# Kernel tuning notes

Measured on AMD Instinct MI355X. Metric: run time of the kernel, lower is better.

The kernel has to match this reference:

```python
import jax, jax.numpy as jnp
import jax.scipy.linalg as jsl
import numpy as np

EPS = 1e-7            # torchvision iou-loss eps
GIOU_THRESHOLD = 0.2
MIN_VARIANCE = 1e-6


def cxcywh_to_xyxy(b):
    cx, cy, w, h = b[..., 0], b[..., 1], b[..., 2], b[..., 3]
    return jnp.stack([cx - 0.5 * w, cy - 0.5 * h, cx + 0.5 * w, cy + 0.5 * h], axis=-1)


def kalman_filtered_boxes(prev_boxes, prev_logits, image_sizes, swp, sws, log_q_diag):
    # scale: [B,1,4] = [w,h,w,h] for denormalization
    scale = jnp.stack([image_sizes[:, 1], image_sizes[:, 0], image_sizes[:, 1], image_sizes[:, 0]], axis=-1)[:, None, :]
    box_abs = prev_boxes * scale                               # [B,Q,4] absolute cxcywh
    conf = jax.nn.softmax(prev_logits, axis=-1).max(axis=-1)   # [B,Q]
    # predict step: P_pred = F P0 F^T + Q  (track-independent 8x8)
    idx = jnp.arange(4)
    F = jnp.eye(8, dtype=box_abs.dtype).at[idx, idx + 4].set(1.0)
    P0 = jnp.diag(jnp.array([100.0] * 4 + [1000.0] * 4, dtype=box_abs.dtype))
    Qm = jnp.diag(jnp.exp(log_q_diag))
    P_pred = F @ P0 @ F.T + Qm                                 # [8,8]
    # detection covariance R per track (DetectionCovarianceGate)
    hc = jnp.maximum(box_abs[..., 3], 1.0)
    std = jnp.stack([swp * hc, swp * hc, sws * hc, sws * hc], axis=-1)
    std = std / jnp.maximum(conf, 1e-6)[..., None]
    std = jnp.maximum(std, 0.1)
    eye4 = jnp.eye(4, dtype=box_abs.dtype)
    R = eye4 * (std ** 2)[..., None, :] + MIN_VARIANCE * eye4  # [B,Q,4,4]
    # innovation covariance, gain via batched Cholesky + triangular solves
    S = P_pred[:4, :4] + R + MIN_VARIANCE * eye4               # [B,Q,4,4]
    L = jnp.linalg.cholesky(S)
    covHT_T = jnp.broadcast_to(P_pred[:, :4].T, S.shape[:-2] + (4, 8))
    y = jsl.solve_triangular(L, covHT_T, lower=True)
    Kt = jsl.solve_triangular(jnp.swapaxes(L, -1, -2), y, lower=False)
    K = jnp.swapaxes(Kt, -1, -2)                               # [B,Q,8,4]
    # state init from the same box + zero velocity -> F @ mean0 = [box; 0]
    mean_pred = jnp.concatenate([box_abs, jnp.zeros_like(box_abs)], axis=-1)  # [B,Q,8]
    innovation = box_abs - mean_pred[..., :4]  # identically zero; kept faithful to original
    mean_new = mean_pred + jnp.einsum('bqij,bqj->bqi', K, innovation)
    return mean_new[..., :4] / scale


def pairwise_giou_loss(p, t):
    # p: [B,Q,4], t: [B,T,4] in xyxy -> [B,Q,T] GIoU loss
    a = p[:, :, None, :]
    b = t[:, None, :, :]
    area_a = (a[..., 2] - a[..., 0]) * (a[..., 3] - a[..., 1])
    area_b = (b[..., 2] - b[..., 0]) * (b[..., 3] - b[..., 1])
    lt = jnp.maximum(a[..., :2], b[..., :2])
    rb = jnp.minimum(a[..., 2:], b[..., 2:])
    wh = jnp.maximum(rb - lt, 0.0)
    inter = wh[..., 0] * wh[..., 1]
    union = area_a + area_b - inter
    iou = inter / (union + EPS)
    ltc = jnp.minimum(a[..., :2], b[..., :2])
    rbc = jnp.maximum(a[..., 2:], b[..., 2:])
    whc = jnp.maximum(rbc - ltc, 0.0)
    area_c = whc[..., 0] * whc[..., 1]
    giou = iou - (area_c - union) / (area_c + EPS)
    return 1.0 - giou


def ciou_loss_mean(p, t):
    # elementwise complete-IoU loss (torchvision semantics), mean-reduced
    x1, y1, x2, y2 = p[..., 0], p[..., 1], p[..., 2], p[..., 3]
    xg1, yg1, xg2, yg2 = t[..., 0], t[..., 1], t[..., 2], t[..., 3]
    iw = jnp.maximum(jnp.minimum(x2, xg2) - jnp.maximum(x1, xg1), 0.0)
    ih = jnp.maximum(jnp.minimum(y2, yg2) - jnp.maximum(y1, yg1), 0.0)
    inter = iw * ih
    union = (x2 - x1) * (y2 - y1) + (xg2 - xg1) * (yg2 - yg1) - inter
    iou = inter / (union + EPS)
    cw = jnp.maximum(x2, xg2) - jnp.minimum(x1, xg1)
    ch = jnp.maximum(y2, yg2) - jnp.minimum(y1, yg1)
    c2 = cw ** 2 + ch ** 2 + EPS
    d2 = ((x1 + x2 - xg1 - xg2) ** 2 + (y1 + y2 - yg1 - yg2) ** 2) / 4.0
    v = (4.0 / (jnp.pi ** 2)) * (jnp.arctan((xg2 - xg1) / (yg2 - yg1)) - jnp.arctan((x2 - x1) / (y2 - y1))) ** 2
    alpha = jax.lax.stop_gradient(v / (1.0 - iou + v + EPS))
    return jnp.mean(1.0 - iou + d2 / c2 + alpha * v)


def _hungarian(cost):
    # O(n^3) shortest-augmenting-path Hungarian (min-cost square assignment).
    # Returns col assignment for rows 0..n-1 (rows are implicitly arange(n)).
    n = cost.shape[0]
    u = np.zeros(n + 1)
    v = np.zeros(n + 1)
    p = np.zeros(n + 1, dtype=np.int64)
    way = np.zeros(n + 1, dtype=np.int64)
    for i in range(1, n + 1):
        p[0] = i
        j0 = 0
        minv = np.full(n + 1, np.inf)
        used = np.zeros(n + 1, dtype=bool)
        while True:
            used[j0] = True
            i0 = p[j0]
            js = np.nonzero(~used)[0]
            js = js[js > 0]
            cur = cost[i0 - 1, js - 1] - u[i0] - v[js]
            upd = cur < minv[js]
            minv[js] = np.minimum(minv[js], cur)
            way[js[upd]] = j0
            j1 = js[int(np.argmin(minv[js]))]
            delta = minv[j1]
            uj = np.nonzero(used)[0]
            u[p[uj]] += delta
            v[uj] -= delta
            minv[js] -= delta
            j0 = j1
            if p[j0] == 0:
                break
        while j0 != 0:
            j1 = way[j0]
            p[j0] = p[j1]
            j0 = j1
    col_of_row = np.empty(n, dtype=np.int64)
    for j in range(1, n + 1):
        col_of_row[p[j] - 1] = j - 1
    return col_of_row


def setup_inputs() -> dict:
    key = jax.random.key(0)
    k = jax.random.split(key, 4)
    B, Q, C = 8, 512, 92
    prev_boxes = jax.random.uniform(k[0], (B, Q, 4), jnp.float32)
    prev_logits = jax.random.normal(k[1], (B, Q, C), jnp.float32)
    curr_boxes = jax.random.uniform(k[2], (B, Q, 4), jnp.float32)
    image_sizes = jax.random.uniform(k[3], (B, 2), jnp.float32) * 800.0 + 480.0
    return {
        'prev_boxes': prev_boxes,
        'prev_logits': prev_logits,
        'curr_boxes': curr_boxes,
        'image_sizes': image_sizes,
        'std_weight_position': jnp.asarray(0.05, jnp.float32),
        'std_weight_size': jnp.asarray(0.05, jnp.float32),
        'log_q_diag': jnp.log(jnp.array([0.01] * 4 + [1e-4] * 4, jnp.float32)),
    }


def reference(prev_boxes, prev_logits, curr_boxes, image_sizes, std_weight_position, std_weight_size, log_q_diag):
    filtered = kalman_filtered_boxes(prev_boxes, prev_logits, image_sizes,
                                     std_weight_position, std_weight_size, log_q_diag)
    # Hungarian matching on thresholded pairwise GIoU-loss cost (no-grad in original)
    gl = pairwise_giou_loss(cxcywh_to_xyxy(curr_boxes), cxcywh_to_xyxy(filtered))  # [B,Q,Q]
    cost = np.asarray(jax.lax.stop_gradient(gl) < GIOU_THRESHOLD, dtype=np.float64)
    cols = jnp.asarray(np.stack([_hungarian(cost[b]) for b in range(cost.shape[0])]))
    # original: matched_preds = pred[col_indices]; matched_targets = target[row_indices] (rows=arange)
    matched_preds = jnp.take_along_axis(curr_boxes, cols[..., None], axis=1)
    matched_targets = filtered
    return ciou_loss_mean(cxcywh_to_xyxy(matched_preds), cxcywh_to_xyxy(matched_targets))
```

## Files before the change

### kernel.cpp

```cpp
#include <hip/hip_runtime.h>
#include <stdint.h>
#include <math.h>

#define NB 8
#define NQ 512

typedef unsigned long long u64;

#define CW(k, r) costL[((k) << 9) + (r)]

static __device__ __forceinline__ u64 getw8(const u64 (&a)[8], int w) {
    u64 r = 0ull;
#pragma unroll
    for (int k = 0; k < 8; k++) if (k == w) r = a[k];
    return r;
}
static __device__ __forceinline__ void setbit8(u64 (&a)[8], int c) {
    int w = c >> 6; u64 m = 1ull << (c & 63);
#pragma unroll
    for (int k = 0; k < 8; k++) if (k == w) a[k] |= m;
}
static __device__ __forceinline__ bool getbit8(const u64 (&a)[8], int c) {
    return (getw8(a, c >> 6) >> (c & 63)) & 1ull;
}

__global__ void cost_kernel(const float* __restrict__ prev_boxes,
                            const float* __restrict__ curr_boxes,
                            const float* __restrict__ image_sizes,
                            u64* __restrict__ cost,
                            float* __restrict__ out) {
#pragma clang fp contract(off)
    int t = blockIdx.x * blockDim.x + threadIdx.x;
    if (t == 0) out[0] = 0.f;
    int b = t >> 18;
    int rem = t & (NQ * NQ - 1);
    int i = rem >> 9;
    int j = rem & (NQ - 1);
    float4 cb = ((const float4*)curr_boxes)[(b << 9) + i];
    float ax = cb.x - 0.5f * cb.z, ay = cb.y - 0.5f * cb.w;
    float az = cb.x + 0.5f * cb.z, aw = cb.y + 0.5f * cb.w;
    float H = image_sizes[2 * b + 0];
    float W = image_sizes[2 * b + 1];
    float4 pb = ((const float4*)prev_boxes)[(b << 9) + j];
    float fcx = (pb.x * W) / W, fcy = (pb.y * H) / H;
    float fw  = (pb.z * W) / W, fh  = (pb.w * H) / H;
    float bx = fcx - 0.5f * fw, by = fcy - 0.5f * fh;
    float bz = fcx + 0.5f * fw, bw = fcy + 0.5f * fh;
    float area_a = (az - ax) * (aw - ay);
    float area_b = (bz - bx) * (bw - by);
    float ltx = fmaxf(ax, bx), lty = fmaxf(ay, by);
    float rbx = fminf(az, bz), rby = fminf(aw, bw);
    float w = fmaxf(rbx - ltx, 0.f), h = fmaxf(rby - lty, 0.f);
    float inter = w * h;
    float uni = area_a + area_b - inter;
    float iou = inter / (uni + 1e-7f);
    float lcx = fminf(ax, bx), lcy = fminf(ay, by);
    float rcx = fmaxf(az, bz), rcy = fmaxf(aw, bw);
    float wc = fmaxf(rcx - lcx, 0.f), hc = fmaxf(rcy - lcy, 0.f);
    float areac = wc * hc;
    float giou = iou - (areac - uni) / (areac + 1e-7f);
    float gl = 1.f - giou;
    u64 m = __ballot(gl < 0.2f);
    if ((threadIdx.x & 63) == 0)
        cost[(size_t)b * (NQ * 8) + ((size_t)(j >> 6) << 9) + i] = m;
}

__global__ __launch_bounds__(256, 1) void hungarian_kernel(
        const u64* __restrict__ cost,
        const float* __restrict__ prev_boxes,
        const float* __restrict__ curr_boxes,
        const float* __restrict__ image_sizes,
        float* __restrict__ out) {
    int b = blockIdx.x;
    int tid = threadIdx.x;
    int lane = tid & 63;
    int wv = tid >> 6;
    __shared__ __align__(16) u64 costL[NQ * 8];
    __shared__ int p[NQ + 1];
    __shared__ int wayL[NQ + 1];
    __shared__ int u[NQ + 1];
    __shared__ int vv[NQ + 1];
    __shared__ int minvA[NQ + 1];
    __shared__ unsigned char used[NQ + 1];
    __shared__ u64 nzS[8], c0S[8], dgS[8], apS[8], zcS[8];
    __shared__ int actionS;
    __shared__ int wIdxS;

    {
        const ulonglong2* src = (const ulonglong2*)(cost + (size_t)b * NQ * 8);
        ulonglong2* dst = (ulonglong2*)costL;
        for (int k = tid; k < NQ * 4; k += 256) dst[k] = src[k];
    }
    for (int k = tid; k <= NQ; k += 256) { p[k] = k; wayL[k] = 0; u[k] = 0; vv[k] = 0; }
    __syncthreads();

#pragma unroll
    for (int gi = 0; gi < 2; gi++) {
        int g = 2 * wv + gi;
        int r = (g << 6) + lane;
        u64 o = 0ull, w0 = 0ull, wg = 0ull;
#pragma unroll
        for (int k = 0; k < 8; k++) {
            u64 x = CW(k, r);
            o |= x;
            if (k == 0) w0 = x;
            if (k == g) wg = x;
        }
        u64 nzb = __ballot(o != 0ull);
        u64 c0b = __ballot((w0 & 1ull) != 0ull);
        u64 dgb = __ballot(((wg >> lane) & 1ull) != 0ull);
        if (lane == 0) { nzS[g] = nzb; c0S[g] = c0b; dgS[g] = dgb; apS[g] = 0ull; }
    }
    __syncthreads();

    u64 nzB[8], c0B[8], dgB[8], apB[8];
    bool ownerNZ0 = false;
    int owner0 = 1;
    u64 Zc[8];
    int wIdx = 0;
    u64 bits = 0ull, pendMask = ~0ull;
    bool started = false;
    if (tid == 0) {
#pragma unroll
        for (int k = 0; k < 8; k++) { nzB[k] = nzS[k]; c0B[k] = c0S[k]; dgB[k] = dgS[k]; apB[k] = 0ull; Zc[k] = 0ull; }
    }

    auto intW = [&](int w) -> u64 {
        u64 x = getw8(c0B, w) | getw8(dgB, w);
        if (ownerNZ0) x |= getw8(apB, w);
        return getw8(nzB, w) & x;
    };
    auto runGeneral = [&](int igen) {
        for (int j = igen; j <= NQ; j++) p[j] = 0;
        for (int i2 = igen; i2 <= NQ; i2++) {
            p[0] = i2;
            for (int j = 0; j <= NQ; j++) { minvA[j] = 0x7fffffff; used[j] = 0; }
            int j0 = 0;
            while (true) {
                used[j0] = 1;
                int i0 = p[j0];
                int ui0 = u[i0];
                int delta = 0x7fffffff, j1 = 0;
                for (int j = 1; j <= NQ; j++) {
                    if (!used[j]) {
                        int cbit = (int)((CW((j - 1) >> 6, i0 - 1) >> ((j - 1) & 63)) & 1ull);
                        int cur = cbit - ui0 - vv[j];
                        if (cur < minvA[j]) { minvA[j] = cur; wayL[j] = (i2 << 10) | j0; }
                        if (minvA[j] < delta) { delta = minvA[j]; j1 = j; }
                    }
                }
                for (int j = 0; j <= NQ; j++) {
                    if (used[j]) { u[p[j]] += delta; vv[j] -= delta; }
                    else minvA[j] -= delta;
                }
                j0 = j1;
                if (p[j0] == 0) break;
            }
            while (j0) {
                int wv2 = wayL[j0];
                int jn = ((wv2 >> 10) == i2) ? (wv2 & 1023) : 0;
                p[j0] = p[jn];
                j0 = jn;
            }
        }
    };

    for (;;) {
        if (tid == 0) {
            int action = 0;
            if (!started) {
                started = true;
                if (nzB[0] & 1ull) {
                    u64 Z1[8];
#pragma unroll
                    for (int k = 0; k < 8; k++) Z1[k] = CW(k, 0);
                    if (!(Z1[0] & 1ull)) {
                        owner0 = 1; ownerNZ0 = true;
#pragma unroll
                        for (int k = 0; k < 8; k++) Zc[k] = Z1[k];
                        action = 1; pendMask = ~1ull; wIdx = 0;
                    } else {
                        runGeneral(1); action = 3;
                    }
                } else {
                    bits = intW(0) & ~1ull;
                }
            }
            while (action == 0) {
                if (bits == 0ull) {
                    wIdx++;
                    if (wIdx >= 8) { action = 3; break; }
                    bits = intW(wIdx);
                    continue;
                }
                int l = __builtin_ctzll(bits);
                bits &= bits - 1;
                u64 rem = (l == 63) ? 0ull : (~0ull << (l + 1));
                int i = (wIdx << 6) + l + 1;
                bool c0 = (getw8(c0B, wIdx) >> l) & 1ull;
                bool apb = ownerNZ0 && ((getw8(apB, wIdx) >> l) & 1ull);
                if (!c0 && !apb) {
                    p[i] = owner0;
                    p[1] = i;
                    owner0 = i; ownerNZ0 = true;
#pragma unroll
                    for (int k = 0; k < 8; k++) Zc[k] = CW(k, i - 1);
                    action = 1; pendMask = rem;
                } else {
                    int prevO = owner0; bool prevF = ownerNZ0;
                    bool bail = false, hole = false;
                    u64 Z[8];
#pragma unroll
                    for (int k = 0; k < 8; k++) Z[k] = CW(k, i - 1);
                    u64 ones[8], vis[8], nzA[8], nzBf[8];
#pragma unroll
                    for (int k = 0; k < 8; k++) { ones[k] = Z[k]; vis[k] = 0ull; nzA[k] = 0ull; nzBf[k] = 0ull; }
                    int fA_c = 0, fA_p = 0, fB_c = 0, fB_p = 0;
                    int foldn = 0, assignTo = -1;
                    while (true) {
                        int c2 = -1;
#pragma unroll
                        for (int k = 7; k >= 0; k--) {
                            u64 s = ~ones[k] & ~vis[k];
                            if (s != 0ull) c2 = (k << 6) + __builtin_ctzll(s);
                        }
                        if (c2 < 0) { bail = true; break; }
                        if (c2 >= i - 1) {
                            if (c2 == i - 1) assignTo = c2;
                            else hole = true;
                            break;
                        }
                        int pc = p[c2 + 1];
                        u64 Zo[8];
#pragma unroll
                        for (int k = 0; k < 8; k++) Zo[k] = CW(k, pc - 1);
                        setbit8(vis, c2);
                        u64 nzv[8], ap2 = 0ull;
#pragma unroll
                        for (int k = 0; k < 8; k++) { nzv[k] = ones[k] & ~Zo[k]; ones[k] &= Zo[k]; ap2 |= ones[k]; }
                        if (foldn == 0) {
                            fA_c = c2; fA_p = pc;
#pragma unroll
                            for (int k = 0; k < 8; k++) nzA[k] = nzv[k];
                        } else if (foldn == 1) {
                            fB_c = c2; fB_p = pc;
#pragma unroll
                            for (int k = 0; k < 8; k++) nzBf[k] = nzv[k];
                        } else {
#pragma unroll
                            for (int k = 0; k < 8; k++) {
                                u64 tt = nzv[k];
                                while (tt) { int b2 = __builtin_ctzll(tt); tt &= tt - 1; wayL[(k << 6) + b2 + 1] = (i << 10) | (c2 + 1); }
                            }
                        }
                        foldn++;
                        if (ap2 == 0ull) { assignTo = i - 1; break; }
                    }
                    if (bail || hole) {
                        runGeneral(i);
                        action = 3;
                    } else {
                        int cc = assignTo;
                        while (true) {
                            bool inA = getbit8(nzA, cc), inB = getbit8(nzBf, cc);
                            if (inB)      { p[cc + 1] = fB_p; cc = fB_c; }
                            else if (inA) { p[cc + 1] = fA_p; cc = fA_c; }
                            else if (foldn > 2) {
                                int wv2 = wayL[cc + 1];
                                if ((wv2 >> 10) == i) { int jn = wv2 & 1023; p[cc + 1] = p[jn]; cc = jn - 1; }
                                else                  { p[cc + 1] = i; break; }
                            } else { p[cc + 1] = i; break; }
                        }
                        owner0 = p[1];
                        ownerNZ0 = (getw8(nzB, (owner0 - 1) >> 6) >> ((owner0 - 1) & 63)) & 1ull;
                        if (ownerNZ0 && !(prevF && prevO == owner0)) {
#pragma unroll
                            for (int k = 0; k < 8; k++) Zc[k] = CW(k, owner0 - 1);
                            action = 1; pendMask = rem;
                        } else {
                            bits = intW(wIdx) & rem;
                        }
                    }
                }
            }
            if (action == 1) {
#pragma unroll
                for (int k = 0; k < 8; k++) zcS[k] = Zc[k];
                wIdxS = wIdx;
            }
            actionS = action;
        }
        __syncthreads();
        int action = actionS;
        if (action == 1) {
            u64 zc[8];
#pragma unroll
            for (int k = 0; k < 8; k++) zc[k] = zcS[k];
            int w0 = wIdxS;
#pragma unroll
            for (int gi = 0; gi < 2; gi++) {
                int g = 2 * wv + gi;
                if (g >= w0) {
                    int r = (g << 6) + lane;
                    u64 a = 0ull;
#pragma unroll
                    for (int k = 0; k < 8; k++) a |= CW(k, r) & zc[k];
                    u64 bal = __ballot(a != 0ull);
                    if (lane == 0) apS[g] = bal;
                }
            }
            __syncthreads();
            if (tid == 0) {
#pragma unroll
                for (int k = 0; k < 8; k++) apB[k] = apS[k];
                ownerNZ0 = true;
                bits = intW(wIdx) & pendMask;
            }
            continue;
        }
        break;
    }
    __syncthreads();

    {
#pragma clang fp contract(off)
        float H = image_sizes[2 * b + 0];
        float W = image_sizes[2 * b + 1];
        float sum = 0.f;
#pragma unroll
        for (int k = 0; k < 2; k++) {
            int j = 1 + tid + (k << 8);
            int r = p[j] - 1;
            int c = j - 1;
            float4 cb = ((const float4*)curr_boxes)[(b << 9) + c];
            float x1 = cb.x - 0.5f * cb.z, y1 = cb.y - 0.5f * cb.w;
            float x2 = cb.x + 0.5f * cb.z, y2 = cb.y + 0.5f * cb.w;
            float4 pb = ((const float4*)prev_boxes)[(b << 9) + r];
            float fcx = (pb.x * W) / W, fcy = (pb.y * H) / H;
            float fw2 = (pb.z * W) / W, fh2 = (pb.w * H) / H;
            float xg1 = fcx - 0.5f * fw2, yg1 = fcy - 0.5f * fh2;
            float xg2 = fcx + 0.5f * fw2, yg2 = fcy + 0.5f * fh2;
            float iw = fmaxf(fminf(x2, xg2) - fmaxf(x1, xg1), 0.f);
            float ih = fmaxf(fminf(y2, yg2) - fmaxf(y1, yg1), 0.f);
            float inter = iw * ih;
            float uni = (x2 - x1) * (y2 - y1) + (xg2 - xg1) * (yg2 - yg1) - inter;
            float iou = inter / (uni + 1e-7f);
            float cw2 = fmaxf(x2, xg2) - fminf(x1, xg1);
            float ch2 = fmaxf(y2, yg2) - fminf(y1, yg1);
            float c2 = cw2 * cw2 + ch2 * ch2 + 1e-7f;
            float dx = ((x1 + x2) - xg1) - xg2;
            float dy = ((y1 + y2) - yg1) - yg2;
            float d2 = (dx * dx + dy * dy) / 4.f;
            const float CC = (float)(4.0 / (M_PI * M_PI));
            float at = atanf((xg2 - xg1) / (yg2 - yg1)) - atanf((x2 - x1) / (y2 - y1));
            float v = CC * (at * at);
            float alpha = v / (((1.f - iou) + v) + 1e-7f);
            sum += ((1.f - iou) + d2 / c2) + alpha * v;
        }
#pragma unroll
        for (int off = 32; off >= 1; off >>= 1) sum += __shfl_xor(sum, off, 64);
        if (lane == 0) atomicAdd(out, sum * (1.f / 4096.f));
    }
}

extern "C" void kernel_launch(void* const* d_in, const int* in_sizes, int n_in,
                              void* d_out, int out_size, void* d_ws, size_t ws_size,
                              hipStream_t stream) {
    const float* prev_boxes  = (const float*)d_in[0];
    const float* curr_boxes  = (const float*)d_in[2];
    const float* image_sizes = (const float*)d_in[3];

    u64* cost = (u64*)d_ws;
    float* out = (float*)d_out;

    cost_kernel<<<(NB * NQ * NQ) / 256, 256, 0, stream>>>(
        prev_boxes, curr_boxes, image_sizes, cost, out);
    hungarian_kernel<<<NB, 256, 0, stream>>>(
        cost, prev_boxes, curr_boxes, image_sizes, out);
}
```

Measured before the change: 78.96 us.

## Run Hungarian fast path in one wavefront and precompute filtered boxes

The Hungarian fast-path control loop now runs entirely inside wavefront 0. Each row group's bitmasks are recomputed with wave ballots in place of the single-thread-plus-block-barrier handshake through shared memory. This is meant to remove repeated __syncthreads round trips and the serialization on thread 0. A new prep kernel computes the filtered xyxy boxes once, so the cost and loss stages no longer redo the per-pair scaling and divisions. The trade-offs are an extra kernel launch and the other three waves sitting idle during matching.

After: 77.72 us. No clear change (-1.6%).

```diff
diff --git a/kernel.cpp b/kernel.cpp
--- a/kernel.cpp
+++ b/kernel.cpp
@@ -24,14 +24,28 @@
     return (getw8(a, c >> 6) >> (c & 63)) & 1ull;
 }
 
-__global__ void cost_kernel(const float* __restrict__ prev_boxes,
-                            const float* __restrict__ curr_boxes,
+__global__ void prep_kernel(const float* __restrict__ prev_boxes,
                             const float* __restrict__ image_sizes,
-                            u64* __restrict__ cost,
+                            float4* __restrict__ filt,
                             float* __restrict__ out) {
 #pragma clang fp contract(off)
     int t = blockIdx.x * blockDim.x + threadIdx.x;
     if (t == 0) out[0] = 0.f;
+    int b = t >> 9;
+    float4 pb = ((const float4*)prev_boxes)[t];
+    float H = image_sizes[2 * b + 0];
+    float W = image_sizes[2 * b + 1];
+    float fcx = (pb.x * W) / W, fcy = (pb.y * H) / H;
+    float fw  = (pb.z * W) / W, fh  = (pb.w * H) / H;
+    filt[t] = make_float4(fcx - 0.5f * fw, fcy - 0.5f * fh,
+                          fcx + 0.5f * fw, fcy + 0.5f * fh);
+}
+
+__global__ void cost_kernel(const float* __restrict__ curr_boxes,
+                            const float4* __restrict__ filt,
+                            u64* __restrict__ cost) {
+#pragma clang fp contract(off)
+    int t = blockIdx.x * blockDim.x + threadIdx.x;
     int b = t >> 18;
     int rem = t & (NQ * NQ - 1);
     int i = rem >> 9;
@@ -39,13 +53,8 @@
     float4 cb = ((const float4*)curr_boxes)[(b << 9) + i];
     float ax = cb.x - 0.5f * cb.z, ay = cb.y - 0.5f * cb.w;
     float az = cb.x + 0.5f * cb.z, aw = cb.y + 0.5f * cb.w;
-    float H = image_sizes[2 * b + 0];
-    float W = image_sizes[2 * b + 1];
-    float4 pb = ((const float4*)prev_boxes)[(b << 9) + j];
-    float fcx = (pb.x * W) / W, fcy = (pb.y * H) / H;
-    float fw  = (pb.z * W) / W, fh  = (pb.w * H) / H;
-    float bx = fcx - 0.5f * fw, by = fcy - 0.5f * fh;
-    float bz = fcx + 0.5f * fw, bw = fcy + 0.5f * fh;
+    float4 fb = filt[(b << 9) + j];
+    float bx = fb.x, by = fb.y, bz = fb.z, bw = fb.w;
     float area_a = (az - ax) * (aw - ay);
     float area_b = (bz - bx) * (bw - by);
     float ltx = fmaxf(ax, bx), lty = fmaxf(ay, by);
@@ -67,9 +76,8 @@
 
 __global__ __launch_bounds__(256, 1) void hungarian_kernel(
         const u64* __restrict__ cost,
-        const float* __restrict__ prev_boxes,
         const float* __restrict__ curr_boxes,
-        const float* __restrict__ image_sizes,
+        const float4* __restrict__ filt,
         float* __restrict__ out) {
     int b = blockIdx.x;
     int tid = threadIdx.x;
@@ -82,9 +90,6 @@
     __shared__ int vv[NQ + 1];
     __shared__ int minvA[NQ + 1];
     __shared__ unsigned char used[NQ + 1];
-    __shared__ u64 nzS[8], c0S[8], dgS[8], apS[8], zcS[8];
-    __shared__ int actionS;
-    __shared__ int wIdxS;
 
     {
         const ulonglong2* src = (const ulonglong2*)(cost + (size_t)b * NQ * 8);
@@ -94,120 +99,88 @@
     for (int k = tid; k <= NQ; k += 256) { p[k] = k; wayL[k] = 0; u[k] = 0; vv[k] = 0; }
     __syncthreads();
 
-#pragma unroll
-    for (int gi = 0; gi < 2; gi++) {
-        int g = 2 * wv + gi;
-        int r = (g << 6) + lane;
-        u64 o = 0ull, w0 = 0ull, wg = 0ull;
-#pragma unroll
-        for (int k = 0; k < 8; k++) {
-            u64 x = CW(k, r);
-            o |= x;
-            if (k == 0) w0 = x;
-            if (k == g) wg = x;
-        }
-        u64 nzb = __ballot(o != 0ull);
-        u64 c0b = __ballot((w0 & 1ull) != 0ull);
-        u64 dgb = __ballot(((wg >> lane) & 1ull) != 0ull);
-        if (lane == 0) { nzS[g] = nzb; c0S[g] = c0b; dgS[g] = dgb; apS[g] = 0ull; }
-    }
-    __syncthreads();
-
-    u64 nzB[8], c0B[8], dgB[8], apB[8];
-    bool ownerNZ0 = false;
-    int owner0 = 1;
-    u64 Zc[8];
-    int wIdx = 0;
-    u64 bits = 0ull, pendMask = ~0ull;
-    bool started = false;
-    if (tid == 0) {
-#pragma unroll
-        for (int k = 0; k < 8; k++) { nzB[k] = nzS[k]; c0B[k] = c0S[k]; dgB[k] = dgS[k]; apB[k] = 0ull; Zc[k] = 0ull; }
-    }
-
-    auto intW = [&](int w) -> u64 {
-        u64 x = getw8(c0B, w) | getw8(dgB, w);
-        if (ownerNZ0) x |= getw8(apB, w);
-        return getw8(nzB, w) & x;
-    };
-    auto runGeneral = [&](int igen) {
-        for (int j = igen; j <= NQ; j++) p[j] = 0;
-        for (int i2 = igen; i2 <= NQ; i2++) {
-            p[0] = i2;
-            for (int j = 0; j <= NQ; j++) { minvA[j] = 0x7fffffff; used[j] = 0; }
-            int j0 = 0;
-            while (true) {
-                used[j0] = 1;
-                int i0 = p[j0];
-                int ui0 = u[i0];
-                int delta = 0x7fffffff, j1 = 0;
-                for (int j = 1; j <= NQ; j++) {
-                    if (!used[j]) {
-                        int cbit = (int)((CW((j - 1) >> 6, i0 - 1) >> ((j - 1) & 63)) & 1ull);
-                        int cur = cbit - ui0 - vv[j];
-                        if (cur < minvA[j]) { minvA[j] = cur; wayL[j] = (i2 << 10) | j0; }
-                        if (minvA[j] < delta) { delta = minvA[j]; j1 = j; }
-                    }
+    if (wv == 0) {
+        auto runGeneral = [&](int igen) {
+            for (int j = igen; j <= NQ; j++) p[j] = 0;
+            for (int i2 = igen; i2 <= NQ; i2++) {
+                p[0] = i2;
+                for (int j = 0; j <= NQ; j++) { minvA[j] = 0x7fffffff; used[j] = 0; }
+                int j0 = 0;
+                while (true) {
+                    used[j0] = 1;
+                    int i0 = p[j0];
+                    int ui0 = u[i0];
+                    int delta = 0x7fffffff, j1 = 0;
+                    for (int j = 1; j <= NQ; j++) {
+                        if (!used[j]) {
+                            int cbit = (int)((CW((j - 1) >> 6, i0 - 1) >> ((j - 1) & 63)) & 1ull);
+                            int cur = cbit - ui0 - vv[j];
+                            if (cur < minvA[j]) { minvA[j] = cur; wayL[j] = (i2 << 10) | j0; }
+                            if (minvA[j] < delta) { delta = minvA[j]; j1 = j; }
+                        }
+                    }
+                    for (int j = 0; j <= NQ; j++) {
+                        if (used[j]) { u[p[j]] += delta; vv[j] -= delta; }
+                        else minvA[j] -= delta;
+                    }
+                    j0 = j1;
+                    if (p[j0] == 0) break;
                 }
-                for (int j = 0; j <= NQ; j++) {
-                    if (used[j]) { u[p[j]] += delta; vv[j] -= delta; }
-                    else minvA[j] -= delta;
-                }
-                j0 = j1;
-                if (p[j0] == 0) break;
-            }
-            while (j0) {
-                int wv2 = wayL[j0];
-                int jn = ((wv2 >> 10) == i2) ? (wv2 & 1023) : 0;
-                p[j0] = p[jn];
-                j0 = jn;
-            }
-        }
-    };
-
-    for (;;) {
-        if (tid == 0) {
-            int action = 0;
-            if (!started) {
-                started = true;
-                if (nzB[0] & 1ull) {
-                    u64 Z1[8];
-#pragma unroll
-                    for (int k = 0; k < 8; k++) Z1[k] = CW(k, 0);
-                    if (!(Z1[0] & 1ull)) {
-                        owner0 = 1; ownerNZ0 = true;
-#pragma unroll
-                        for (int k = 0; k < 8; k++) Zc[k] = Z1[k];
-                        action = 1; pendMask = ~1ull; wIdx = 0;
-                    } else {
-                        runGeneral(1); action = 3;
-                    }
-                } else {
-                    bits = intW(0) & ~1ull;
+                while (j0) {
+                    int wv2 = wayL[j0];
+                    int jn = ((wv2 >> 10) == i2) ? (wv2 & 1023) : 0;
+                    p[j0] = p[jn];
+                    j0 = jn;
                 }
             }
-            while (action == 0) {
-                if (bits == 0ull) {
-                    wIdx++;
-                    if (wIdx >= 8) { action = 3; break; }
-                    bits = intW(wIdx);
-                    continue;
+        };
+
+        u64 Zc[8];
+#pragma unroll
+        for (int k = 0; k < 8; k++) Zc[k] = 0ull;
+        int owner0 = 1;
+        bool done = false;
+
+        for (int g = 0; g < 8 && !done; g++) {
+            u64 R[8];
+            int r = (g << 6) + lane;
+#pragma unroll
+            for (int k = 0; k < 8; k++) R[k] = CW(k, r);
+            u64 orR = 0ull;
+#pragma unroll
+            for (int k = 0; k < 8; k++) orR |= R[k];
+            u64 nzw = __ballot(orR != 0ull);
+            u64 c0w = __ballot((R[0] & 1ull) != 0ull);
+            u64 dgw = __ballot(((getw8(R, g) >> lane) & 1ull) != 0ull);
+
+            if (g == 0) {
+                if ((nzw & c0w) & 1ull) {
+                    if (lane == 0) runGeneral(1);
+                    done = true;
+                    break;
                 }
+#pragma unroll
+                for (int k = 0; k < 8; k++) Zc[k] = CW(k, 0);
+            }
+            u64 ao = 0ull;
+#pragma unroll
+            for (int k = 0; k < 8; k++) ao |= (R[k] & Zc[k]);
+            u64 apw = __ballot(ao != 0ull);
+            u64 bits = nzw & (c0w | dgw | apw);
+            if (g == 0) bits &= ~1ull;
+
+            while (bits) {
                 int l = __builtin_ctzll(bits);
-                bits &= bits - 1;
                 u64 rem = (l == 63) ? 0ull : (~0ull << (l + 1));
-                int i = (wIdx << 6) + l + 1;
-                bool c0 = (getw8(c0B, wIdx) >> l) & 1ull;
-                bool apb = ownerNZ0 && ((getw8(apB, wIdx) >> l) & 1ull);
+                int i = (g << 6) + l + 1;
+                bool c0 = (c0w >> l) & 1ull;
+                bool apb = (apw >> l) & 1ull;
                 if (!c0 && !apb) {
-                    p[i] = owner0;
-                    p[1] = i;
-                    owner0 = i; ownerNZ0 = true;
+                    if (lane == 0) { p[i] = owner0; p[1] = i; }
+                    owner0 = i;
 #pragma unroll
                     for (int k = 0; k < 8; k++) Zc[k] = CW(k, i - 1);
-                    action = 1; pendMask = rem;
                 } else {
-                    int prevO = owner0; bool prevF = ownerNZ0;
                     bool bail = false, hole = false;
                     u64 Z[8];
 #pragma unroll
@@ -247,85 +220,49 @@
 #pragma unroll
                             for (int k = 0; k < 8; k++) nzBf[k] = nzv[k];
                         } else {
-#pragma unroll
-                            for (int k = 0; k < 8; k++) {
-                                u64 tt = nzv[k];
-                                while (tt) { int b2 = __builtin_ctzll(tt); tt &= tt - 1; wayL[(k << 6) + b2 + 1] = (i << 10) | (c2 + 1); }
+                            if (lane == 0) {
+#pragma unroll
+                                for (int k = 0; k < 8; k++) {
+                                    u64 tt = nzv[k];
+                                    while (tt) { int b2 = __builtin_ctzll(tt); tt &= tt - 1; wayL[(k << 6) + b2 + 1] = (i << 10) | (c2 + 1); }
+                                }
                             }
                         }
                         foldn++;
                         if (ap2 == 0ull) { assignTo = i - 1; break; }
                     }
                     if (bail || hole) {
-                        runGeneral(i);
-                        action = 3;
-                    } else {
-                        int cc = assignTo;
-                        while (true) {
-                            bool inA = getbit8(nzA, cc), inB = getbit8(nzBf, cc);
-                            if (inB)      { p[cc + 1] = fB_p; cc = fB_c; }
-                            else if (inA) { p[cc + 1] = fA_p; cc = fA_c; }
-                            else if (foldn > 2) {
-                                int wv2 = wayL[cc + 1];
-                                if ((wv2 >> 10) == i) { int jn = wv2 & 1023; p[cc + 1] = p[jn]; cc = jn - 1; }
-                                else                  { p[cc + 1] = i; break; }
-                            } else { p[cc + 1] = i; break; }
-                        }
-                        owner0 = p[1];
-                        ownerNZ0 = (getw8(nzB, (owner0 - 1) >> 6) >> ((owner0 - 1) & 63)) & 1ull;
-                        if (ownerNZ0 && !(prevF && prevO == owner0)) {
-#pragma unroll
-                            for (int k = 0; k < 8; k++) Zc[k] = CW(k, owner0 - 1);
-                            action = 1; pendMask = rem;
-                        } else {
-                            bits = intW(wIdx) & rem;
-                        }
-                    }
+                        if (lane == 0) runGeneral(i);
+                        done = true;
+                        break;
+                    }
+                    int cc = assignTo;
+                    while (true) {
+                        bool inA = getbit8(nzA, cc), inB = getbit8(nzBf, cc);
+                        if (inB)      { if (lane == 0) p[cc + 1] = fB_p; cc = fB_c; }
+                        else if (inA) { if (lane == 0) p[cc + 1] = fA_p; cc = fA_c; }
+                        else if (foldn > 2) {
+                            int wv2 = wayL[cc + 1];
+                            if ((wv2 >> 10) == i) { int jn = wv2 & 1023; int pv = p[jn]; if (lane == 0) p[cc + 1] = pv; cc = jn - 1; }
+                            else                  { if (lane == 0) p[cc + 1] = i; break; }
+                        } else { if (lane == 0) p[cc + 1] = i; break; }
+                    }
+                    owner0 = p[1];
+#pragma unroll
+                    for (int k = 0; k < 8; k++) Zc[k] = CW(k, owner0 - 1);
                 }
+                u64 ao2 = 0ull;
+#pragma unroll
+                for (int k = 0; k < 8; k++) ao2 |= (R[k] & Zc[k]);
+                apw = __ballot(ao2 != 0ull);
+                bits = nzw & (c0w | dgw | apw) & rem;
             }
-            if (action == 1) {
-#pragma unroll
-                for (int k = 0; k < 8; k++) zcS[k] = Zc[k];
-                wIdxS = wIdx;
-            }
-            actionS = action;
         }
-        __syncthreads();
-        int action = actionS;
-        if (action == 1) {
-            u64 zc[8];
-#pragma unroll
-            for (int k = 0; k < 8; k++) zc[k] = zcS[k];
-            int w0 = wIdxS;
-#pragma unroll
-            for (int gi = 0; gi < 2; gi++) {
-                int g = 2 * wv + gi;
-                if (g >= w0) {
-                    int r = (g << 6) + lane;
-                    u64 a = 0ull;
-#pragma unroll
-                    for (int k = 0; k < 8; k++) a |= CW(k, r) & zc[k];
-                    u64 bal = __ballot(a != 0ull);
-                    if (lane == 0) apS[g] = bal;
-                }
-            }
-            __syncthreads();
-            if (tid == 0) {
-#pragma unroll
-                for (int k = 0; k < 8; k++) apB[k] = apS[k];
-                ownerNZ0 = true;
-                bits = intW(wIdx) & pendMask;
-            }
-            continue;
-        }
-        break;
     }
     __syncthreads();
 
     {
 #pragma clang fp contract(off)
-        float H = image_sizes[2 * b + 0];
-        float W = image_sizes[2 * b + 1];
         float sum = 0.f;
 #pragma unroll
         for (int k = 0; k < 2; k++) {
@@ -335,11 +272,8 @@
             float4 cb = ((const float4*)curr_boxes)[(b << 9) + c];
             float x1 = cb.x - 0.5f * cb.z, y1 = cb.y - 0.5f * cb.w;
             float x2 = cb.x + 0.5f * cb.z, y2 = cb.y + 0.5f * cb.w;
-            float4 pb = ((const float4*)prev_boxes)[(b << 9) + r];
-            float fcx = (pb.x * W) / W, fcy = (pb.y * H) / H;
-            float fw2 = (pb.z * W) / W, fh2 = (pb.w * H) / H;
-            float xg1 = fcx - 0.5f * fw2, yg1 = fcy - 0.5f * fh2;
-            float xg2 = fcx + 0.5f * fw2, yg2 = fcy + 0.5f * fh2;
+            float4 fb = filt[(b << 9) + r];
+            float xg1 = fb.x, yg1 = fb.y, xg2 = fb.z, yg2 = fb.w;
             float iw = fmaxf(fminf(x2, xg2) - fmaxf(x1, xg1), 0.f);
             float ih = fmaxf(fminf(y2, yg2) - fmaxf(y1, yg1), 0.f);
             float inter = iw * ih;
@@ -370,11 +304,14 @@
     const float* curr_boxes  = (const float*)d_in[2];
     const float* image_sizes = (const float*)d_in[3];
 
-    u64* cost = (u64*)d_ws;
+    float4* filt = (float4*)d_ws;
+    u64* cost = (u64*)((char*)d_ws + 65536);
     float* out = (float*)d_out;
 
+    prep_kernel<<<(NB * NQ) / 256, 256, 0, stream>>>(
+        prev_boxes, image_sizes, filt, out);
     cost_kernel<<<(NB * NQ * NQ) / 256, 256, 0, stream>>>(
-        prev_boxes, curr_boxes, image_sizes, cost, out);
+        curr_boxes, filt, cost);
     hungarian_kernel<<<NB, 256, 0, stream>>>(
-        cost, prev_boxes, curr_boxes, image_sizes, out);
-}
+        cost, curr_boxes, filt, out);
+}
```
